# Optimization experiments

Measured on AMD Instinct MI355X. Metric: run time of the kernel, lower is better.

Reference implementation:

```python
import jax, jax.numpy as jnp
import numpy as np

R_MAX = 1.0
BASIS_MASK = 0xFF        # low 8 bits -> basis index (basis_size=256)
R_BITS_MASK = 0xFFFF     # next 16 bits -> quantized radius
R_DENOM = 65535.0
INT8_DENOM = 127.0


def setup_inputs() -> dict:
    key = jax.random.key(0)
    k_x, k_c, k_b, k_r, k_s, k_bias = jax.random.split(key, 6)
    B, S, D_in, D_out, BASIS = 4, 2048, 4096, 4096, 256
    x = jax.random.normal(k_x, (B, S, D_in), dtype=jnp.float32)
    codes = jax.random.randint(k_c, (D_out,), 0, 16777216, dtype=jnp.int32)
    basis_table = jax.random.normal(k_b, (BASIS, D_in), dtype=jnp.float32)
    residual_q = jax.random.randint(k_r, (D_out, D_in), 0, 256, dtype=jnp.int32)
    residual_scales = jax.random.uniform(k_s, (D_out,), dtype=jnp.float32) * 0.05
    bias = jax.random.normal(k_bias, (D_out,), dtype=jnp.float32)
    return {"x": x, "codes": codes, "basis_table": basis_table,
            "residual_q": residual_q, "residual_scales": residual_scales,
            "bias": bias}


def decode_weight(codes, basis_table, residual_q, residual_scales):
    # Bitfield decode: low 8 bits = basis index, next 16 bits = quantized radius in [0, r_max].
    idx = codes & BASIS_MASK                                   # [O]
    r = ((codes >> 8) & R_BITS_MASK).astype(jnp.float32) / R_DENOM * R_MAX  # [O]
    base = r[:, None] * basis_table[idx]                       # [O, I]
    resid = (residual_q.astype(jnp.float32) - 128.0) / INT8_DENOM  # dequant int8 residual
    return base + residual_scales[:, None] * resid             # [O, I]


def reference(x, codes, basis_table, residual_q, residual_scales, bias):
    W = decode_weight(codes, basis_table, residual_q, residual_scales)  # [O, I]
    # y = x @ W^T + bias  (fused dequant-matmul in the original CUDA kernel)
    return jnp.einsum("bsi,oi->bso", x, W) + bias
```

## Files before the change

### kernel.cpp

```cpp
#include <hip/hip_runtime.h>


typedef __bf16 bf16x8 __attribute__((ext_vector_type(8)));
typedef float f32x4 __attribute__((ext_vector_type(4)));
typedef int i32x4 __attribute__((ext_vector_type(4)));
typedef unsigned short u16x8 __attribute__((ext_vector_type(8)));

__device__ __forceinline__ unsigned short f2bf(float f) {
    union { float f; unsigned int u; } c; c.f = f;
    unsigned int u = c.u;
    u += 0x7fffu + ((u >> 16) & 1u);
    return (unsigned short)(u >> 16);
}
__device__ __forceinline__ float bf2f(unsigned short h) {
    union { unsigned int u; float f; } c; c.u = ((unsigned int)h) << 16;
    return c.f;
}

__device__ __forceinline__ void load_lds16(const void* g, void* l) {
    __builtin_amdgcn_global_load_lds(
        (__attribute__((address_space(1))) void*)(void*)g,
        (__attribute__((address_space(3))) void*)l,
        16, 0, 0);
}

__device__ __forceinline__ int swz_decode(int p, int row_bytes) {
    const int g = p >> 3, t = p & 7, v = t ^ (g & 7);
    const int row = g * 2 + (v >> 2), chunk = v & 3;
    return row * row_bytes + chunk * 16;
}

__global__ void cvt_bf16_kernel(const float4* __restrict__ in4,
                                ushort4* __restrict__ out4, int n4) {
    int i = blockIdx.x * blockDim.x + threadIdx.x;
    const int stride = gridDim.x * blockDim.x;
    for (; i < n4; i += stride) {
        float4 v = in4[i];
        ushort4 o;
        o.x = f2bf(v.x); o.y = f2bf(v.y); o.z = f2bf(v.z); o.w = f2bf(v.w);
        out4[i] = o;
    }
}

__global__ void quant_x_kernel(const float* __restrict__ x,
                               signed char* __restrict__ xq,
                               float* __restrict__ arow, int K) {
    const int m = blockIdx.x;
    const float* row = x + (size_t)m * K;
    const int base = threadIdx.x * 16;
    float4 v[4];
#pragma unroll
    for (int j = 0; j < 4; ++j) v[j] = *(const float4*)(row + base + j * 4);

    float lmax = 0.f;
#pragma unroll
    for (int j = 0; j < 4; ++j) {
        lmax = fmaxf(lmax, fabsf(v[j].x));
        lmax = fmaxf(lmax, fabsf(v[j].y));
        lmax = fmaxf(lmax, fabsf(v[j].z));
        lmax = fmaxf(lmax, fabsf(v[j].w));
    }
#pragma unroll
    for (int off = 32; off; off >>= 1)
        lmax = fmaxf(lmax, __shfl_xor(lmax, off));
    __shared__ float smax[4];
    if ((threadIdx.x & 63) == 0) smax[threadIdx.x >> 6] = lmax;
    __syncthreads();
    const float mx = fmaxf(fmaxf(smax[0], smax[1]), fmaxf(smax[2], smax[3]));
    const float inv = mx > 0.f ? 127.0f / mx : 0.0f;
    if (threadIdx.x == 0) arow[m] = mx * (1.0f / 127.0f);

    union { signed char c[16]; i32x4 w; } pk;
#pragma unroll
    for (int j = 0; j < 4; ++j) {
        pk.c[j * 4 + 0] = (signed char)(int)rintf(v[j].x * inv);
        pk.c[j * 4 + 1] = (signed char)(int)rintf(v[j].y * inv);
        pk.c[j * 4 + 2] = (signed char)(int)rintf(v[j].z * inv);
        pk.c[j * 4 + 3] = (signed char)(int)rintf(v[j].w * inv);
    }
    *(i32x4*)(xq + (size_t)m * K + base) = pk.w;
}

__global__ void pack_q_kernel(const int4* __restrict__ q4,
                              unsigned int* __restrict__ out, int n4) {
    const int i = blockIdx.x * blockDim.x + threadIdx.x;
    if (i >= n4) return;
    int4 a = q4[i];
    unsigned int w = ((unsigned)(a.x - 128) & 0xFFu)
                   | (((unsigned)(a.y - 128) & 0xFFu) << 8)
                   | (((unsigned)(a.z - 128) & 0xFFu) << 16)
                   | (((unsigned)(a.w - 128) & 0xFFu) << 24);
    out[i] = w;
}

__global__ __launch_bounds__(256) void
p_gemm_kernel(const float* __restrict__ x,
              const unsigned short* __restrict__ Bb,
              unsigned short* __restrict__ Pbf,
              int M, int K) {
    __shared__ __align__(16) float As[32 * 64];
    __shared__ __align__(16) unsigned short Bs[256 * 64];

    const int tid  = threadIdx.x;
    const int lane = tid & 63;
    const int wv   = tid >> 6;
    const int m0 = blockIdx.x * 32;
    const int lr = lane & 15;
    const int kg = lane >> 4;

    f32x4 acc[2][4];
#pragma unroll
    for (int mi = 0; mi < 2; ++mi)
#pragma unroll
        for (int ni = 0; ni < 4; ++ni)
            acc[mi][ni] = (f32x4){0.f, 0.f, 0.f, 0.f};

    int aRow[2], aSrc[2];
#pragma unroll
    for (int j = 0; j < 2; ++j) {
        const int p = tid + 256 * j;
        aRow[j] = p >> 4;
        aSrc[j] = (p & 15) ^ (aRow[j] & 15);
    }
    int bRow[8], bSrc[8];
#pragma unroll
    for (int j = 0; j < 8; ++j) {
        const int p = tid + 256 * j;
        bRow[j] = p >> 3;
        bSrc[j] = (p & 7) ^ (bRow[j] & 7);
    }

    for (int k0 = 0; k0 < K; k0 += 64) {
#pragma unroll
        for (int j = 0; j < 2; ++j)
            load_lds16(x + (size_t)(m0 + aRow[j]) * K + k0 + aSrc[j] * 4,
                       (char*)As + (tid + 256 * j) * 16);
#pragma unroll
        for (int j = 0; j < 8; ++j)
            load_lds16(Bb + (size_t)bRow[j] * K + k0 + bSrc[j] * 8,
                       (char*)Bs + (tid + 256 * j) * 16);
        __syncthreads();

#pragma unroll
        for (int s = 0; s < 2; ++s) {
            bf16x8 af[2];
#pragma unroll
            for (int mi = 0; mi < 2; ++mi) {
                const int r = mi * 16 + lr;
                const int c0 = s * 8 + kg * 2;
                const int ph0 = c0 ^ (r & 15);
                const int ph1 = (c0 + 1) ^ (r & 15);
                f32x4 lo = *(const f32x4*)(As + r * 64 + ph0 * 4);
                f32x4 hi = *(const f32x4*)(As + r * 64 + ph1 * 4);
                bf16x8 a;
                a[0] = (__bf16)lo[0]; a[1] = (__bf16)lo[1];
                a[2] = (__bf16)lo[2]; a[3] = (__bf16)lo[3];
                a[4] = (__bf16)hi[0]; a[5] = (__bf16)hi[1];
                a[6] = (__bf16)hi[2]; a[7] = (__bf16)hi[3];
                af[mi] = a;
            }
#pragma unroll
            for (int ni = 0; ni < 4; ++ni) {
                const int rb = wv * 64 + ni * 16 + lr;
                const int ph = (s * 4 + kg) ^ (rb & 7);
                bf16x8 bfr = __builtin_bit_cast(bf16x8,
                    *(const u16x8*)(Bs + rb * 64 + ph * 8));
#pragma unroll
                for (int mi = 0; mi < 2; ++mi)
                    acc[mi][ni] = __builtin_amdgcn_mfma_f32_16x16x32_bf16(
                        af[mi], bfr, acc[mi][ni], 0, 0, 0);
            }
        }
        __syncthreads();
    }

#pragma unroll
    for (int ni = 0; ni < 4; ++ni) {
        const int n = wv * 64 + ni * 16 + lr;
#pragma unroll
        for (int mi = 0; mi < 2; ++mi) {
            const int mbase = m0 + mi * 16 + kg * 4;
#pragma unroll
            for (int rg = 0; rg < 4; ++rg)
                Pbf[(size_t)(mbase + rg) * 256 + n] = f2bf(acc[mi][ni][rg]);
        }
    }
}

__global__ __launch_bounds__(256, 2) void
gemm_i8_kernel(const signed char* __restrict__ Xq,
               const signed char* __restrict__ Qb,
               const float* __restrict__ arow,
               const int* __restrict__ codes,
               const float* __restrict__ scales,
               const float* __restrict__ bias,
               const unsigned short* __restrict__ Pbf,
               float* __restrict__ out,
               int M, int N, int K) {
    __shared__ __align__(16) signed char As[128 * 64];
    __shared__ __align__(16) signed char Bs[256 * 64];

    const int tid  = threadIdx.x;
    const int lane = tid & 63;
    const int wv   = tid >> 6;
    const int wr   = wv >> 1;
    const int wc   = wv & 1;
    const int m0 = blockIdx.x * 128;
    const int n0 = blockIdx.y * 256;
    const int lr = lane & 15;
    const int kg = lane >> 4;
    const int cidx = (((lr & 1) << 2) | kg) ^ ((lr >> 1) & 7);

    i32x4 acc[4][8];
#pragma unroll
    for (int mi = 0; mi < 4; ++mi)
#pragma unroll
        for (int ni = 0; ni < 8; ++ni)
            acc[mi][ni] = (i32x4){0, 0, 0, 0};

    int gaOff[2], gbOff[4];
#pragma unroll
    for (int j = 0; j < 2; ++j) gaOff[j] = swz_decode(tid + 256 * j, 64);
#pragma unroll
    for (int j = 0; j < 4; ++j) gbOff[j] = swz_decode(tid + 256 * j, 64);

    for (int k0 = 0; k0 < K; k0 += 64) {
#pragma unroll
        for (int j = 0; j < 2; ++j)
            load_lds16(Xq + (size_t)(m0 + (gaOff[j] >> 6)) * K + (gaOff[j] & 63) + k0,
                       As + (tid + 256 * j) * 16);
#pragma unroll
        for (int j = 0; j < 4; ++j)
            load_lds16(Qb + (size_t)(n0 + (gbOff[j] >> 6)) * K + (gbOff[j] & 63) + k0,
                       Bs + (tid + 256 * j) * 16);
        __syncthreads();

        i32x4 af[4], bfr[8];
#pragma unroll
        for (int mi = 0; mi < 4; ++mi) {
            const int r2 = wr * 32 + mi * 8 + (lr >> 1);
            af[mi] = *(const i32x4*)(As + r2 * 128 + cidx * 16);
        }
#pragma unroll
        for (int ni = 0; ni < 8; ++ni) {
            const int r2 = wc * 64 + ni * 8 + (lr >> 1);
            bfr[ni] = *(const i32x4*)(Bs + r2 * 128 + cidx * 16);
        }
#pragma unroll
        for (int mi = 0; mi < 4; ++mi)
#pragma unroll
            for (int ni = 0; ni < 8; ++ni)
                acc[mi][ni] = __builtin_amdgcn_mfma_i32_16x16x64_i8(
                    af[mi], bfr[ni], acc[mi][ni], 0, 0, 0);
        __syncthreads();
    }

    float av[4][4];
#pragma unroll
    for (int mi = 0; mi < 4; ++mi)
#pragma unroll
        for (int rg = 0; rg < 4; ++rg)
            av[mi][rg] = arow[m0 + wr * 64 + mi * 16 + kg * 4 + rg];

#pragma unroll
    for (int ni = 0; ni < 8; ++ni) {
        const int n = n0 + wc * 128 + ni * 16 + lr;
        const int code = codes[n];
        const int cc = code & 0xFF;
        const float rr = (float)((code >> 8) & 0xFFFF) * (1.0f / 65535.0f);
        const float so = scales[n] * (1.0f / 127.0f);
        const float bv = bias[n];
#pragma unroll
        for (int mi = 0; mi < 4; ++mi) {
            const int mbase = m0 + wr * 64 + mi * 16 + kg * 4;
            unsigned short pv[4];
#pragma unroll
            for (int rg = 0; rg < 4; ++rg)
                pv[rg] = Pbf[(size_t)(mbase + rg) * 256 + cc];
#pragma unroll
            for (int rg = 0; rg < 4; ++rg) {
                const float y = av[mi][rg] * so * (float)acc[mi][ni][rg]
                              + rr * bf2f(pv[rg]) + bv;
                __builtin_nontemporal_store(y, &out[(size_t)(mbase + rg) * N + n]);
            }
        }
    }
}

extern "C" void kernel_launch(void* const* d_in, const int* in_sizes, int n_in,
                              void* d_out, int out_size, void* d_ws, size_t ws_size,
                              hipStream_t stream) {
    const float* x        = (const float*)d_in[0];
    const int*   codes    = (const int*)d_in[1];
    const float* basis    = (const float*)d_in[2];
    const int*   q        = (const int*)d_in[3];
    const float* scales   = (const float*)d_in[4];
    const float* bias     = (const float*)d_in[5];
    float* out = (float*)d_out;

    const int BASIS = 256;
    const int K = in_sizes[2] / BASIS;
    const int N = in_sizes[1];
    const int M = in_sizes[0] / K;

    char* ws = (char*)d_ws;
    signed char* Xq = (signed char*)ws;
    size_t off = (size_t)M * K;
    signed char* Qb = (signed char*)(ws + off);
    off += (size_t)N * K;
    unsigned short* Pbf = (unsigned short*)(ws + off);
    off += (size_t)M * 256 * 2;
    float* Arow = (float*)(ws + off);
    off += (size_t)M * sizeof(float);
    unsigned short* Bb = (unsigned short*)(ws + off);

    cvt_bf16_kernel<<<1024, 256, 0, stream>>>((const float4*)basis, (ushort4*)Bb,
                                              BASIS * K / 4);
    p_gemm_kernel<<<M / 32, 256, 0, stream>>>(x, Bb, Pbf, M, K);
    quant_x_kernel<<<M, 256, 0, stream>>>(x, Xq, Arow, K);
    pack_q_kernel<<<(N * K / 4 + 255) / 256, 256, 0, stream>>>(
        (const int4*)q, (unsigned int*)Qb, N * K / 4);
    gemm_i8_kernel<<<dim3(M / 128, N / 256), 256, 0, stream>>>(
        Xq, Qb, Arow, codes, scales, bias, Pbf, out, M, N, K);
}
```

Baseline: 498.6 us.

## Double-buffer LDS and enlarge int8 GEMM tile to 256x256 with 512 threads

Rewrites the int8 main GEMM to use 256x256 tiles with 8 waves, a 128-wide K step split into two halves, and a double-buffered 128KB LDS region. Global-to-LDS prefetch of the next tile is interleaved between MFMA phases, using explicit waitcnt, barriers and setprio. The small P GEMM also moves to 512 threads with double buffering. The aim is to hide global load latency and raise MFMA density per LDS read. In exchange, the large LDS footprint limits occupancy and the hand-placed waitcnt counts carry correctness risk.

```diff
diff --git a/kernel.cpp b/kernel.cpp
--- a/kernel.cpp
+++ b/kernel.cpp
@@ -93,101 +93,100 @@
     out[i] = w;
 }
 
-__global__ __launch_bounds__(256) void
+__global__ __launch_bounds__(512) void
 p_gemm_kernel(const float* __restrict__ x,
               const unsigned short* __restrict__ Bb,
               unsigned short* __restrict__ Pbf,
               int M, int K) {
-    __shared__ __align__(16) float As[32 * 64];
-    __shared__ __align__(16) unsigned short Bs[256 * 64];
+    __shared__ __align__(16) float As[2][32 * 64];
+    __shared__ __align__(16) unsigned short Bs[2][256 * 64];
 
     const int tid  = threadIdx.x;
     const int lane = tid & 63;
     const int wv   = tid >> 6;
+    const int wr   = wv >> 2;
+    const int wc   = wv & 3;
     const int m0 = blockIdx.x * 32;
     const int lr = lane & 15;
     const int kg = lane >> 4;
 
-    f32x4 acc[2][4];
-#pragma unroll
-    for (int mi = 0; mi < 2; ++mi)
-#pragma unroll
-        for (int ni = 0; ni < 4; ++ni)
-            acc[mi][ni] = (f32x4){0.f, 0.f, 0.f, 0.f};
-
-    int aRow[2], aSrc[2];
-#pragma unroll
-    for (int j = 0; j < 2; ++j) {
-        const int p = tid + 256 * j;
-        aRow[j] = p >> 4;
-        aSrc[j] = (p & 15) ^ (aRow[j] & 15);
-    }
-    int bRow[8], bSrc[8];
-#pragma unroll
-    for (int j = 0; j < 8; ++j) {
-        const int p = tid + 256 * j;
+    f32x4 acc[4];
+#pragma unroll
+    for (int ni = 0; ni < 4; ++ni) acc[ni] = (f32x4){0.f, 0.f, 0.f, 0.f};
+
+    const int aRow = tid >> 4;
+    const int aSrc = (tid & 15) ^ (aRow & 15);
+    int bRow[4], bSrc[4];
+#pragma unroll
+    for (int j = 0; j < 4; ++j) {
+        const int p = tid + 512 * j;
         bRow[j] = p >> 3;
         bSrc[j] = (p & 7) ^ (bRow[j] & 7);
     }
-
-    for (int k0 = 0; k0 < K; k0 += 64) {
-#pragma unroll
-        for (int j = 0; j < 2; ++j)
-            load_lds16(x + (size_t)(m0 + aRow[j]) * K + k0 + aSrc[j] * 4,
-                       (char*)As + (tid + 256 * j) * 16);
-#pragma unroll
-        for (int j = 0; j < 8; ++j)
-            load_lds16(Bb + (size_t)bRow[j] * K + k0 + bSrc[j] * 8,
-                       (char*)Bs + (tid + 256 * j) * 16);
-        __syncthreads();
-
+    const float* aG = x + (size_t)(m0 + aRow) * K + aSrc * 4;
+    const unsigned short* bG[4];
+#pragma unroll
+    for (int j = 0; j < 4; ++j) bG[j] = Bb + (size_t)bRow[j] * K + bSrc[j] * 8;
+
+#define P_STAGE(bb, k0)                                                        \
+    do {                                                                       \
+        load_lds16(aG + (k0), (char*)As[bb] + tid * 16);                       \
+        _Pragma("unroll") for (int j = 0; j < 4; ++j)                          \
+            load_lds16(bG[j] + (k0), (char*)Bs[bb] + (tid + 512 * j) * 16);    \
+    } while (0)
+
+    P_STAGE(0, 0);
+    const int NT = K >> 6;
+    for (int t = 0; t < NT; ++t) {
+        const int bb = t & 1;
+        if (t + 1 < NT) {
+            P_STAGE(bb ^ 1, (t + 1) << 6);
+            asm volatile("s_waitcnt vmcnt(5)" ::: "memory");
+        } else {
+            asm volatile("s_waitcnt vmcnt(0)" ::: "memory");
+        }
+        __builtin_amdgcn_s_barrier();
+
+        const float* Ab = As[bb];
+        const unsigned short* Bbf = Bs[bb];
 #pragma unroll
         for (int s = 0; s < 2; ++s) {
-            bf16x8 af[2];
-#pragma unroll
-            for (int mi = 0; mi < 2; ++mi) {
-                const int r = mi * 16 + lr;
-                const int c0 = s * 8 + kg * 2;
-                const int ph0 = c0 ^ (r & 15);
-                const int ph1 = (c0 + 1) ^ (r & 15);
-                f32x4 lo = *(const f32x4*)(As + r * 64 + ph0 * 4);
-                f32x4 hi = *(const f32x4*)(As + r * 64 + ph1 * 4);
-                bf16x8 a;
-                a[0] = (__bf16)lo[0]; a[1] = (__bf16)lo[1];
-                a[2] = (__bf16)lo[2]; a[3] = (__bf16)lo[3];
-                a[4] = (__bf16)hi[0]; a[5] = (__bf16)hi[1];
-                a[6] = (__bf16)hi[2]; a[7] = (__bf16)hi[3];
-                af[mi] = a;
-            }
+            const int r = wr * 16 + lr;
+            const int c0 = s * 8 + kg * 2;
+            const int ph0 = c0 ^ (r & 15);
+            const int ph1 = (c0 + 1) ^ (r & 15);
+            f32x4 lo = *(const f32x4*)(Ab + r * 64 + ph0 * 4);
+            f32x4 hi = *(const f32x4*)(Ab + r * 64 + ph1 * 4);
+            bf16x8 a;
+            a[0] = (__bf16)lo[0]; a[1] = (__bf16)lo[1];
+            a[2] = (__bf16)lo[2]; a[3] = (__bf16)lo[3];
+            a[4] = (__bf16)hi[0]; a[5] = (__bf16)hi[1];
+            a[6] = (__bf16)hi[2]; a[7] = (__bf16)hi[3];
 #pragma unroll
             for (int ni = 0; ni < 4; ++ni) {
-                const int rb = wv * 64 + ni * 16 + lr;
+                const int rb = wc * 64 + ni * 16 + lr;
                 const int ph = (s * 4 + kg) ^ (rb & 7);
                 bf16x8 bfr = __builtin_bit_cast(bf16x8,
-                    *(const u16x8*)(Bs + rb * 64 + ph * 8));
-#pragma unroll
-                for (int mi = 0; mi < 2; ++mi)
-                    acc[mi][ni] = __builtin_amdgcn_mfma_f32_16x16x32_bf16(
-                        af[mi], bfr, acc[mi][ni], 0, 0, 0);
+                    *(const u16x8*)(Bbf + rb * 64 + ph * 8));
+                acc[ni] = __builtin_amdgcn_mfma_f32_16x16x32_bf16(
+                    a, bfr, acc[ni], 0, 0, 0);
             }
         }
-        __syncthreads();
-    }
+        __builtin_amdgcn_s_barrier();
+    }
+#undef P_STAGE
 
 #pragma unroll
     for (int ni = 0; ni < 4; ++ni) {
-        const int n = wv * 64 + ni * 16 + lr;
-#pragma unroll
-        for (int mi = 0; mi < 2; ++mi) {
-            const int mbase = m0 + mi * 16 + kg * 4;
-#pragma unroll
-            for (int rg = 0; rg < 4; ++rg)
-                Pbf[(size_t)(mbase + rg) * 256 + n] = f2bf(acc[mi][ni][rg]);
-        }
-    }
-}
-
-__global__ __launch_bounds__(256, 2) void
+        const int n = wc * 64 + ni * 16 + lr;
+        const int mb = m0 + wr * 16 + kg * 4;
+#pragma unroll
+        for (int rg = 0; rg < 4; ++rg)
+            Pbf[(size_t)(mb + rg) * 256 + n] = f2bf(acc[ni][rg]);
+    }
+}
+
+__global__ __launch_bounds__(512, 2) void
 gemm_i8_kernel(const signed char* __restrict__ Xq,
                const signed char* __restrict__ Qb,
                const float* __restrict__ arow,
@@ -197,82 +196,163 @@
                const unsigned short* __restrict__ Pbf,
                float* __restrict__ out,
                int M, int N, int K) {
-    __shared__ __align__(16) signed char As[128 * 64];
-    __shared__ __align__(16) signed char Bs[256 * 64];
+    __shared__ __align__(16) signed char lds[2 * 65536];
 
     const int tid  = threadIdx.x;
     const int lane = tid & 63;
     const int wv   = tid >> 6;
-    const int wr   = wv >> 1;
-    const int wc   = wv & 1;
-    const int m0 = blockIdx.x * 128;
+    const int wr   = wv >> 2;
+    const int wc   = wv & 3;
+    const int m0 = blockIdx.x * 256;
     const int n0 = blockIdx.y * 256;
     const int lr = lane & 15;
     const int kg = lane >> 4;
     const int cidx = (((lr & 1) << 2) | kg) ^ ((lr >> 1) & 7);
 
-    i32x4 acc[4][8];
-#pragma unroll
-    for (int mi = 0; mi < 4; ++mi)
-#pragma unroll
-        for (int ni = 0; ni < 8; ++ni)
+    const int o0 = swz_decode(tid, 64);
+    const int o1 = swz_decode(tid + 512, 64);
+    const signed char* aG0 = Xq + (size_t)(m0 + (o0 >> 6)) * K + (o0 & 63);
+    const signed char* aG1 = Xq + (size_t)(m0 + (o1 >> 6)) * K + (o1 & 63);
+    const signed char* bG0 = Qb + (size_t)(n0 + (o0 >> 6)) * K + (o0 & 63);
+    const signed char* bG1 = Qb + (size_t)(n0 + (o1 >> 6)) * K + (o1 & 63);
+    const int d0 = tid * 16;
+    const int d1 = d0 + 8192;
+
+    i32x4 acc[8][4];
+#pragma unroll
+    for (int mi = 0; mi < 8; ++mi)
+#pragma unroll
+        for (int ni = 0; ni < 4; ++ni)
             acc[mi][ni] = (i32x4){0, 0, 0, 0};
 
-    int gaOff[2], gbOff[4];
-#pragma unroll
-    for (int j = 0; j < 2; ++j) gaOff[j] = swz_decode(tid + 256 * j, 64);
-#pragma unroll
-    for (int j = 0; j < 4; ++j) gbOff[j] = swz_decode(tid + 256 * j, 64);
-
-    for (int k0 = 0; k0 < K; k0 += 64) {
-#pragma unroll
-        for (int j = 0; j < 2; ++j)
-            load_lds16(Xq + (size_t)(m0 + (gaOff[j] >> 6)) * K + (gaOff[j] & 63) + k0,
-                       As + (tid + 256 * j) * 16);
-#pragma unroll
-        for (int j = 0; j < 4; ++j)
-            load_lds16(Qb + (size_t)(n0 + (gbOff[j] >> 6)) * K + (gbOff[j] & 63) + k0,
-                       Bs + (tid + 256 * j) * 16);
-        __syncthreads();
-
-        i32x4 af[4], bfr[8];
-#pragma unroll
-        for (int mi = 0; mi < 4; ++mi) {
-            const int r2 = wr * 32 + mi * 8 + (lr >> 1);
-            af[mi] = *(const i32x4*)(As + r2 * 128 + cidx * 16);
-        }
-#pragma unroll
-        for (int ni = 0; ni < 8; ++ni) {
-            const int r2 = wc * 64 + ni * 8 + (lr >> 1);
-            bfr[ni] = *(const i32x4*)(Bs + r2 * 128 + cidx * 16);
-        }
-#pragma unroll
-        for (int mi = 0; mi < 4; ++mi)
-#pragma unroll
-            for (int ni = 0; ni < 8; ++ni)
-                acc[mi][ni] = __builtin_amdgcn_mfma_i32_16x16x64_i8(
-                    af[mi], bfr[ni], acc[mi][ni], 0, 0, 0);
-        __syncthreads();
-    }
-
-    float av[4][4];
-#pragma unroll
-    for (int mi = 0; mi < 4; ++mi)
+    const int raBase = (wr * 64 + (lr >> 1)) * 128 + cidx * 16;
+    const int rbBase = 32768 + (wc * 32 + (lr >> 1)) * 128 + cidx * 16;
+
+#define STG_A(bufo, ks, kb)                                                    \
+    do {                                                                       \
+        load_lds16(aG0 + (kb) + (ks) * 64, lds + (bufo) + (ks) * 16384 + d0);  \
+        load_lds16(aG1 + (kb) + (ks) * 64, lds + (bufo) + (ks) * 16384 + d1);  \
+    } while (0)
+#define STG_B(bufo, ks, kb)                                                    \
+    do {                                                                       \
+        load_lds16(bG0 + (kb) + (ks) * 64,                                     \
+                   lds + (bufo) + 32768 + (ks) * 16384 + d0);                  \
+        load_lds16(bG1 + (kb) + (ks) * 64,                                     \
+                   lds + (bufo) + 32768 + (ks) * 16384 + d1);                  \
+    } while (0)
+
+    STG_A(0, 0, 0); STG_B(0, 0, 0); STG_A(0, 1, 0); STG_B(0, 1, 0);
+    asm volatile("s_waitcnt vmcnt(4)" ::: "memory");
+    __builtin_amdgcn_s_barrier();
+
+    const int NT = K >> 7;
+#pragma unroll 2
+    for (int t = 0; t < NT; ++t) {
+        const int buf  = (t & 1) << 16;
+        const int nbuf = buf ^ 65536;
+        const int kb   = (t + 1) << 7;
+        const bool pre = (t + 1) < NT;
+        i32x4 a[8], b0, b1;
+
+#pragma unroll
+        for (int mi = 0; mi < 8; ++mi)
+            a[mi] = *(const i32x4*)(lds + buf + raBase + mi * 1024);
+        b0 = *(const i32x4*)(lds + buf + rbBase + 0 * 1024);
+        b1 = *(const i32x4*)(lds + buf + rbBase + 1 * 1024);
+        if (pre) STG_A(nbuf, 0, kb);
+        __builtin_amdgcn_s_barrier();
+        asm volatile("s_waitcnt lgkmcnt(0)" ::: "memory");
+        __builtin_amdgcn_s_setprio(1);
+#pragma unroll
+        for (int mi = 0; mi < 8; ++mi)
+            acc[mi][0] = __builtin_amdgcn_mfma_i32_16x16x64_i8(a[mi], b0,
+                                                               acc[mi][0], 0, 0, 0);
+#pragma unroll
+        for (int mi = 0; mi < 8; ++mi)
+            acc[mi][1] = __builtin_amdgcn_mfma_i32_16x16x64_i8(a[mi], b1,
+                                                               acc[mi][1], 0, 0, 0);
+        __builtin_amdgcn_s_setprio(0);
+        __builtin_amdgcn_s_barrier();
+
+        b0 = *(const i32x4*)(lds + buf + rbBase + 2 * 1024);
+        b1 = *(const i32x4*)(lds + buf + rbBase + 3 * 1024);
+        if (pre) STG_B(nbuf, 0, kb);
+        __builtin_amdgcn_s_barrier();
+        asm volatile("s_waitcnt lgkmcnt(0)" ::: "memory");
+        __builtin_amdgcn_s_setprio(1);
+#pragma unroll
+        for (int mi = 0; mi < 8; ++mi)
+            acc[mi][2] = __builtin_amdgcn_mfma_i32_16x16x64_i8(a[mi], b0,
+                                                               acc[mi][2], 0, 0, 0);
+#pragma unroll
+        for (int mi = 0; mi < 8; ++mi)
+            acc[mi][3] = __builtin_amdgcn_mfma_i32_16x16x64_i8(a[mi], b1,
+                                                               acc[mi][3], 0, 0, 0);
+        __builtin_amdgcn_s_setprio(0);
+        if (pre) asm volatile("s_waitcnt vmcnt(4)" ::: "memory");
+        else     asm volatile("s_waitcnt vmcnt(0)" ::: "memory");
+        __builtin_amdgcn_s_barrier();
+
+#pragma unroll
+        for (int mi = 0; mi < 8; ++mi)
+            a[mi] = *(const i32x4*)(lds + buf + 16384 + raBase + mi * 1024);
+        b0 = *(const i32x4*)(lds + buf + 16384 + rbBase + 0 * 1024);
+        b1 = *(const i32x4*)(lds + buf + 16384 + rbBase + 1 * 1024);
+        if (pre) STG_A(nbuf, 1, kb);
+        __builtin_amdgcn_s_barrier();
+        asm volatile("s_waitcnt lgkmcnt(0)" ::: "memory");
+        __builtin_amdgcn_s_setprio(1);
+#pragma unroll
+        for (int mi = 0; mi < 8; ++mi)
+            acc[mi][0] = __builtin_amdgcn_mfma_i32_16x16x64_i8(a[mi], b0,
+                                                               acc[mi][0], 0, 0, 0);
+#pragma unroll
+        for (int mi = 0; mi < 8; ++mi)
+            acc[mi][1] = __builtin_amdgcn_mfma_i32_16x16x64_i8(a[mi], b1,
+                                                               acc[mi][1], 0, 0, 0);
+        __builtin_amdgcn_s_setprio(0);
+        __builtin_amdgcn_s_barrier();
+
+        b0 = *(const i32x4*)(lds + buf + 16384 + rbBase + 2 * 1024);
+        b1 = *(const i32x4*)(lds + buf + 16384 + rbBase + 3 * 1024);
+        if (pre) STG_B(nbuf, 1, kb);
+        __builtin_amdgcn_s_barrier();
+        asm volatile("s_waitcnt lgkmcnt(0)" ::: "memory");
+        __builtin_amdgcn_s_setprio(1);
+#pragma unroll
+        for (int mi = 0; mi < 8; ++mi)
+            acc[mi][2] = __builtin_amdgcn_mfma_i32_16x16x64_i8(a[mi], b0,
+                                                               acc[mi][2], 0, 0, 0);
+#pragma unroll
+        for (int mi = 0; mi < 8; ++mi)
+            acc[mi][3] = __builtin_amdgcn_mfma_i32_16x16x64_i8(a[mi], b1,
+                                                               acc[mi][3], 0, 0, 0);
+        __builtin_amdgcn_s_setprio(0);
+        if (pre) asm volatile("s_waitcnt vmcnt(4)" ::: "memory");
+        __builtin_amdgcn_s_barrier();
+    }
+#undef STG_A
+#undef STG_B
+
+    const int mwb = m0 + wr * 128 + kg * 4;
+    float av[8][4];
+#pragma unroll
+    for (int mi = 0; mi < 8; ++mi)
 #pragma unroll
         for (int rg = 0; rg < 4; ++rg)
-            av[mi][rg] = arow[m0 + wr * 64 + mi * 16 + kg * 4 + rg];
-
-#pragma unroll
-    for (int ni = 0; ni < 8; ++ni) {
-        const int n = n0 + wc * 128 + ni * 16 + lr;
+            av[mi][rg] = arow[mwb + mi * 16 + rg];
+
+#pragma unroll
+    for (int ni = 0; ni < 4; ++ni) {
+        const int n = n0 + wc * 64 + ni * 16 + lr;
         const int code = codes[n];
         const int cc = code & 0xFF;
         const float rr = (float)((code >> 8) & 0xFFFF) * (1.0f / 65535.0f);
         const float so = scales[n] * (1.0f / 127.0f);
         const float bv = bias[n];
 #pragma unroll
-        for (int mi = 0; mi < 4; ++mi) {
-            const int mbase = m0 + wr * 64 + mi * 16 + kg * 4;
+        for (int mi = 0; mi < 8; ++mi) {
+            const int mbase = mwb + mi * 16;
             unsigned short pv[4];
 #pragma unroll
             for (int rg = 0; rg < 4; ++rg)
@@ -316,10 +396,10 @@
 
     cvt_bf16_kernel<<<1024, 256, 0, stream>>>((const float4*)basis, (ushort4*)Bb,
                                               BASIS * K / 4);
-    p_gemm_kernel<<<M / 32, 256, 0, stream>>>(x, Bb, Pbf, M, K);
+    p_gemm_kernel<<<M / 32, 512, 0, stream>>>(x, Bb, Pbf, M, K);
     quant_x_kernel<<<M, 256, 0, stream>>>(x, Xq, Arow, K);
     pack_q_kernel<<<(N * K / 4 + 255) / 256, 256, 0, stream>>>(
         (const int4*)q, (unsigned int*)Qb, N * K / 4);
-    gemm_i8_kernel<<<dim3(M / 128, N / 256), 256, 0, stream>>>(
+    gemm_i8_kernel<<<dim3(M / 256, N / 256), 512, 0, stream>>>(
         Xq, Qb, Arow, codes, scales, bias, Pbf, out, M, N, K);
 }
```

Result: slower. 522.5 us (+4.8%).

## Double-buffer LDS tiles in both GEMMs and widen the basis-projection kernel to 512 threads

Applied to the files above, without the earlier changes.

Both the basis-projection bf16 GEMM and the main int8 GEMM now use two LDS buffers, so the global-to-LDS loads for the next K tile are issued before computing on the current one. Explicit vmcnt waits and raw barriers replace the two __syncthreads per iteration. The projection kernel also moves to 512 threads, with 8 waves each owning a 16x64 output tile, so the A-tile float-to-bf16 conversion is spread across more waves. The int8 kernel's LDS footprint doubles to 48KB per block under launch bounds of 2 blocks per CU, which may reduce occupancy.

```diff
diff --git a/kernel.cpp b/kernel.cpp
--- a/kernel.cpp
+++ b/kernel.cpp
@@ -93,97 +93,96 @@
     out[i] = w;
 }
 
-__global__ __launch_bounds__(256) void
+__global__ __launch_bounds__(512) void
 p_gemm_kernel(const float* __restrict__ x,
               const unsigned short* __restrict__ Bb,
               unsigned short* __restrict__ Pbf,
               int M, int K) {
-    __shared__ __align__(16) float As[32 * 64];
-    __shared__ __align__(16) unsigned short Bs[256 * 64];
+    __shared__ __align__(16) float As[2][32 * 64];
+    __shared__ __align__(16) unsigned short Bs[2][256 * 64];
 
     const int tid  = threadIdx.x;
     const int lane = tid & 63;
     const int wv   = tid >> 6;
+    const int wr   = wv >> 2;
+    const int wc   = wv & 3;
     const int m0 = blockIdx.x * 32;
     const int lr = lane & 15;
     const int kg = lane >> 4;
 
-    f32x4 acc[2][4];
-#pragma unroll
-    for (int mi = 0; mi < 2; ++mi)
-#pragma unroll
-        for (int ni = 0; ni < 4; ++ni)
-            acc[mi][ni] = (f32x4){0.f, 0.f, 0.f, 0.f};
-
-    int aRow[2], aSrc[2];
-#pragma unroll
-    for (int j = 0; j < 2; ++j) {
-        const int p = tid + 256 * j;
-        aRow[j] = p >> 4;
-        aSrc[j] = (p & 15) ^ (aRow[j] & 15);
-    }
-    int bRow[8], bSrc[8];
-#pragma unroll
-    for (int j = 0; j < 8; ++j) {
-        const int p = tid + 256 * j;
+    f32x4 acc[4];
+#pragma unroll
+    for (int ni = 0; ni < 4; ++ni) acc[ni] = (f32x4){0.f, 0.f, 0.f, 0.f};
+
+    const int aRow = tid >> 4;
+    const int aSrc = (tid & 15) ^ (aRow & 15);
+    int bRow[4], bSrc[4];
+#pragma unroll
+    for (int j = 0; j < 4; ++j) {
+        const int p = tid + 512 * j;
         bRow[j] = p >> 3;
         bSrc[j] = (p & 7) ^ (bRow[j] & 7);
     }
-
-    for (int k0 = 0; k0 < K; k0 += 64) {
-#pragma unroll
-        for (int j = 0; j < 2; ++j)
-            load_lds16(x + (size_t)(m0 + aRow[j]) * K + k0 + aSrc[j] * 4,
-                       (char*)As + (tid + 256 * j) * 16);
-#pragma unroll
-        for (int j = 0; j < 8; ++j)
-            load_lds16(Bb + (size_t)bRow[j] * K + k0 + bSrc[j] * 8,
-                       (char*)Bs + (tid + 256 * j) * 16);
-        __syncthreads();
-
+    const float* aG = x + (size_t)(m0 + aRow) * K + aSrc * 4;
+    const unsigned short* bG[4];
+#pragma unroll
+    for (int j = 0; j < 4; ++j) bG[j] = Bb + (size_t)bRow[j] * K + bSrc[j] * 8;
+
+#define P_STAGE(bb, k0)                                                        \
+    do {                                                                       \
+        load_lds16(aG + (k0), (char*)As[bb] + tid * 16);                       \
+        _Pragma("unroll") for (int j = 0; j < 4; ++j)                          \
+            load_lds16(bG[j] + (k0), (char*)Bs[bb] + (tid + 512 * j) * 16);    \
+    } while (0)
+
+    P_STAGE(0, 0);
+    const int NT = K >> 6;
+    for (int t = 0; t < NT; ++t) {
+        const int bb = t & 1;
+        if (t + 1 < NT) {
+            P_STAGE(bb ^ 1, (t + 1) << 6);
+            asm volatile("s_waitcnt vmcnt(5)" ::: "memory");
+        } else {
+            asm volatile("s_waitcnt vmcnt(0)" ::: "memory");
+        }
+        __builtin_amdgcn_s_barrier();
+
+        const float* Ab = As[bb];
+        const unsigned short* Bbf = Bs[bb];
 #pragma unroll
         for (int s = 0; s < 2; ++s) {
-            bf16x8 af[2];
-#pragma unroll
-            for (int mi = 0; mi < 2; ++mi) {
-                const int r = mi * 16 + lr;
-                const int c0 = s * 8 + kg * 2;
-                const int ph0 = c0 ^ (r & 15);
-                const int ph1 = (c0 + 1) ^ (r & 15);
-                f32x4 lo = *(const f32x4*)(As + r * 64 + ph0 * 4);
-                f32x4 hi = *(const f32x4*)(As + r * 64 + ph1 * 4);
-                bf16x8 a;
-                a[0] = (__bf16)lo[0]; a[1] = (__bf16)lo[1];
-                a[2] = (__bf16)lo[2]; a[3] = (__bf16)lo[3];
-                a[4] = (__bf16)hi[0]; a[5] = (__bf16)hi[1];
-                a[6] = (__bf16)hi[2]; a[7] = (__bf16)hi[3];
-                af[mi] = a;
-            }
+            const int r = wr * 16 + lr;
+            const int c0 = s * 8 + kg * 2;
+            const int ph0 = c0 ^ (r & 15);
+            const int ph1 = (c0 + 1) ^ (r & 15);
+            f32x4 lo = *(const f32x4*)(Ab + r * 64 + ph0 * 4);
+            f32x4 hi = *(const f32x4*)(Ab + r * 64 + ph1 * 4);
+            bf16x8 a;
+            a[0] = (__bf16)lo[0]; a[1] = (__bf16)lo[1];
+            a[2] = (__bf16)lo[2]; a[3] = (__bf16)lo[3];
+            a[4] = (__bf16)hi[0]; a[5] = (__bf16)hi[1];
+            a[6] = (__bf16)hi[2]; a[7] = (__bf16)hi[3];
 #pragma unroll
             for (int ni = 0; ni < 4; ++ni) {
-                const int rb = wv * 64 + ni * 16 + lr;
+                const int rb = wc * 64 + ni * 16 + lr;
                 const int ph = (s * 4 + kg) ^ (rb & 7);
                 bf16x8 bfr = __builtin_bit_cast(bf16x8,
-                    *(const u16x8*)(Bs + rb * 64 + ph * 8));
-#pragma unroll
-                for (int mi = 0; mi < 2; ++mi)
-                    acc[mi][ni] = __builtin_amdgcn_mfma_f32_16x16x32_bf16(
-                        af[mi], bfr, acc[mi][ni], 0, 0, 0);
+                    *(const u16x8*)(Bbf + rb * 64 + ph * 8));
+                acc[ni] = __builtin_amdgcn_mfma_f32_16x16x32_bf16(
+                    a, bfr, acc[ni], 0, 0, 0);
             }
         }
-        __syncthreads();
-    }
+        __builtin_amdgcn_s_barrier();
+    }
+#undef P_STAGE
 
 #pragma unroll
     for (int ni = 0; ni < 4; ++ni) {
-        const int n = wv * 64 + ni * 16 + lr;
-#pragma unroll
-        for (int mi = 0; mi < 2; ++mi) {
-            const int mbase = m0 + mi * 16 + kg * 4;
-#pragma unroll
-            for (int rg = 0; rg < 4; ++rg)
-                Pbf[(size_t)(mbase + rg) * 256 + n] = f2bf(acc[mi][ni][rg]);
-        }
+        const int n = wc * 64 + ni * 16 + lr;
+        const int mb = m0 + wr * 16 + kg * 4;
+#pragma unroll
+        for (int rg = 0; rg < 4; ++rg)
+            Pbf[(size_t)(mb + rg) * 256 + n] = f2bf(acc[ni][rg]);
     }
 }
 
@@ -197,8 +196,8 @@
                const unsigned short* __restrict__ Pbf,
                float* __restrict__ out,
                int M, int N, int K) {
-    __shared__ __align__(16) signed char As[128 * 64];
-    __shared__ __align__(16) signed char Bs[256 * 64];
+    __shared__ __align__(16) signed char As[2][128 * 64];
+    __shared__ __align__(16) signed char Bs[2][256 * 64];
 
     const int tid  = threadIdx.x;
     const int lane = tid & 63;
@@ -224,27 +223,43 @@
 #pragma unroll
     for (int j = 0; j < 4; ++j) gbOff[j] = swz_decode(tid + 256 * j, 64);
 
-    for (int k0 = 0; k0 < K; k0 += 64) {
-#pragma unroll
-        for (int j = 0; j < 2; ++j)
-            load_lds16(Xq + (size_t)(m0 + (gaOff[j] >> 6)) * K + (gaOff[j] & 63) + k0,
-                       As + (tid + 256 * j) * 16);
-#pragma unroll
-        for (int j = 0; j < 4; ++j)
-            load_lds16(Qb + (size_t)(n0 + (gbOff[j] >> 6)) * K + (gbOff[j] & 63) + k0,
-                       Bs + (tid + 256 * j) * 16);
-        __syncthreads();
+    const signed char* aSrc[2];
+    const signed char* bSrc[4];
+#pragma unroll
+    for (int j = 0; j < 2; ++j)
+        aSrc[j] = Xq + (size_t)(m0 + (gaOff[j] >> 6)) * K + (gaOff[j] & 63);
+#pragma unroll
+    for (int j = 0; j < 4; ++j)
+        bSrc[j] = Qb + (size_t)(n0 + (gbOff[j] >> 6)) * K + (gbOff[j] & 63);
+
+#define G_STAGE(bb, k0)                                                        \
+    do {                                                                       \
+        _Pragma("unroll") for (int j = 0; j < 2; ++j)                          \
+            load_lds16(aSrc[j] + (k0), (char*)As[bb] + (tid + 256 * j) * 16);  \
+        _Pragma("unroll") for (int j = 0; j < 4; ++j)                          \
+            load_lds16(bSrc[j] + (k0), (char*)Bs[bb] + (tid + 256 * j) * 16);  \
+    } while (0)
+
+    G_STAGE(0, 0);
+    asm volatile("s_waitcnt vmcnt(0)" ::: "memory");
+    __builtin_amdgcn_s_barrier();
+
+    const int NT = K >> 6;
+#pragma unroll 2
+    for (int t = 0; t < NT; ++t) {
+        const int bb = t & 1;
+        if (t + 1 < NT) G_STAGE(bb ^ 1, (t + 1) << 6);
 
         i32x4 af[4], bfr[8];
 #pragma unroll
         for (int mi = 0; mi < 4; ++mi) {
             const int r2 = wr * 32 + mi * 8 + (lr >> 1);
-            af[mi] = *(const i32x4*)(As + r2 * 128 + cidx * 16);
+            af[mi] = *(const i32x4*)(As[bb] + r2 * 128 + cidx * 16);
         }
 #pragma unroll
         for (int ni = 0; ni < 8; ++ni) {
             const int r2 = wc * 64 + ni * 8 + (lr >> 1);
-            bfr[ni] = *(const i32x4*)(Bs + r2 * 128 + cidx * 16);
+            bfr[ni] = *(const i32x4*)(Bs[bb] + r2 * 128 + cidx * 16);
         }
 #pragma unroll
         for (int mi = 0; mi < 4; ++mi)
@@ -252,8 +267,11 @@
             for (int ni = 0; ni < 8; ++ni)
                 acc[mi][ni] = __builtin_amdgcn_mfma_i32_16x16x64_i8(
                     af[mi], bfr[ni], acc[mi][ni], 0, 0, 0);
-        __syncthreads();
-    }
+
+        asm volatile("s_waitcnt vmcnt(0)" ::: "memory");
+        __builtin_amdgcn_s_barrier();
+    }
+#undef G_STAGE
 
     float av[4][4];
 #pragma unroll
@@ -316,7 +334,7 @@
 
     cvt_bf16_kernel<<<1024, 256, 0, stream>>>((const float4*)basis, (ushort4*)Bb,
                                               BASIS * K / 4);
-    p_gemm_kernel<<<M / 32, 256, 0, stream>>>(x, Bb, Pbf, M, K);
+    p_gemm_kernel<<<M / 32, 512, 0, stream>>>(x, Bb, Pbf, M, K);
     quant_x_kernel<<<M, 256, 0, stream>>>(x, Xq, Arow, K);
     pack_q_kernel<<<(N * K / 4 + 255) / 256, 256, 0, stream>>>(
         (const int4*)q, (unsigned int*)Qb, N * K / 4);
```

New measurement: 493.0 us. No clear change (-1.1%).
